# Optimization experiments

Measured on AMD Instinct MI355X. Metric: run time of the kernel, lower is better.

## Reference

```python
import jax, jax.numpy as jnp
import numpy as np

BATCH = 1_000_000
D = 20

def setup_inputs() -> dict:
    key = jax.random.key(0)
    kX, kW, kb, kR = jax.random.split(key, 4)
    X = jax.random.normal(kX, (BATCH, D), dtype=jnp.float32)
    W = jax.random.normal(kW, (D, D), dtype=jnp.float32)
    b = jax.random.normal(kb, (D,), dtype=jnp.float32)
    rand_weight = jax.random.uniform(kR, (D, D), dtype=jnp.float32)  # torch.rand, requires_grad=False
    return {"X": X, "W": W, "b": b, "rand_weight": rand_weight}

def reference(X, W, b, rand_weight):
    # X = self.linear(X)
    X1 = X @ W.T + b
    # X = relu(X @ rand_weight + 1)
    X2 = jax.nn.relu(X1 @ rand_weight + 1.0)
    # X = self.linear(X)  (shared weights)
    X3 = X2 @ W.T + b
    # while X.abs().sum() > 1: X = X / 2  -- data-dependent loop, kept on-device
    def cond(Xc):
        return jnp.sum(jnp.abs(Xc)) > 1.0
    def body(Xc):
        return Xc * 0.5
    Xf = jax.lax.while_loop(cond, body, X3)
    return jnp.sum(Xf)
```

## Files before the change

kernel.cpp:

```cpp
#include <hip/hip_runtime.h>
#include <math.h>

#define D 20
#define NROWS 1000000
#define NTILES (NROWS / 16)
#define TPB 256
#define MAIN_BLOCKS 1024
#define WAVES_TOTAL (MAIN_BLOCKS * (TPB/64))

typedef float  f32x4  __attribute__((ext_vector_type(4)));
typedef __bf16 bf16x8 __attribute__((ext_vector_type(8)));

#define FRAG_OFF (MAIN_BLOCKS * 2 * 8)

__device__ inline unsigned int pk2(float a, float b) {
  unsigned short la = __builtin_bit_cast(unsigned short, (__bf16)a);
  unsigned short lb = __builtin_bit_cast(unsigned short, (__bf16)b);
  return (unsigned int)la | ((unsigned int)lb << 16);
}

__global__ __launch_bounds__(512) void setup_kernel(
    const float* __restrict__ W, const float* __restrict__ b,
    const float* __restrict__ R, unsigned int* __restrict__ frags) {
  __shared__ float A_s[D * D];
  __shared__ float c_s[D];
  const int t = threadIdx.x;
  if (t < D * D) {
    int j = t / D, m = t % D;
    float s = 0.f;
#pragma unroll
    for (int i = 0; i < D; ++i) s = fmaf(W[i * D + j], R[i * D + m], s);
    A_s[j * D + m] = s;
  } else if (t < D * D + D) {
    int m = t - D * D;
    float s = 1.0f;
#pragma unroll
    for (int i = 0; i < D; ++i) s = fmaf(b[i], R[i * D + m], s);
    c_s[m] = s;
  }
  __syncthreads();
  if (t < 64) {
    const int G = t >> 4, ii = t & 15;
    uint4* out = (uint4*)frags;
    unsigned w[4];
    for (int wd = 0; wd < 4; ++wd) {
      float v[2];
      for (int h = 0; h < 2; ++h) {
        int k = G * 8 + 2 * wd + h;
        v[h] = (k < D) ? A_s[k * D + ii] : (k == D ? c_s[ii] : 0.f);
      }
      w[wd] = pk2(v[0], v[1]);
    }
    out[t] = make_uint4(w[0], w[1], w[2], w[3]);
    for (int wd = 0; wd < 4; ++wd) {
      float v[2];
      for (int h = 0; h < 2; ++h) {
        int k = G * 8 + 2 * wd + h;
        int m = 16 + ii;
        v[h] = (m < D) ? ((k < D) ? A_s[k * D + m] : (k == D ? c_s[m] : 0.f)) : 0.f;
      }
      w[wd] = pk2(v[0], v[1]);
    }
    out[64 + t] = make_uint4(w[0], w[1], w[2], w[3]);
    for (int wd = 0; wd < 4; ++wd) {
      float v[2];
      for (int h = 0; h < 2; ++h) {
        int e = 2 * wd + h;
        int sg = (e < 4) ? (4 * G + e) : (16 + 4 * G + (e - 4));
        v[h] = (sg < D) ? W[ii * D + sg] : (sg == D ? b[ii] : 0.f);
      }
      w[wd] = pk2(v[0], v[1]);
    }
    out[128 + t] = make_uint4(w[0], w[1], w[2], w[3]);
    for (int wd = 0; wd < 4; ++wd) {
      float v[2];
      for (int h = 0; h < 2; ++h) {
        int e = 2 * wd + h;
        int sg = (e < 4) ? (4 * G + e) : (16 + 4 * G + (e - 4));
        int n = 16 + ii;
        v[h] = (n < D) ? ((sg < D) ? W[n * D + sg] : (sg == D ? b[n] : 0.f)) : 0.f;
      }
      w[wd] = pk2(v[0], v[1]);
    }
    out[192 + t] = make_uint4(w[0], w[1], w[2], w[3]);
  }
}

__global__ __launch_bounds__(TPB) void main_kernel(
    const float* __restrict__ X, const unsigned int* __restrict__ frags,
    double* __restrict__ partial) {
  const int tid = threadIdx.x;
  const int lane = tid & 63;
  const int G = lane >> 4, ii = lane & 15;
  const int wid = tid >> 6;
  const int gwave = blockIdx.x * (TPB / 64) + wid;

  const uint4* fr = (const uint4*)frags;
  const bf16x8 B1t1 = __builtin_bit_cast(bf16x8, fr[lane]);
  const bf16x8 B1t2 = __builtin_bit_cast(bf16x8, fr[64 + lane]);
  const bf16x8 B2t1 = __builtin_bit_cast(bf16x8, fr[128 + lane]);
  const bf16x8 B2t2 = __builtin_bit_cast(bf16x8, fr[192 + lane]);

  const int g8 = (G < 2) ? G * 8 : 16;
  double s64 = 0.0, sa64 = 0.0;

  float4 xa = {0.f, 0.f, 0.f, 0.f}, xb = {0.f, 0.f, 0.f, 0.f};
  if (gwave < NTILES) {
    const float* p = X + (size_t)(gwave * 16 + ii) * D + g8;
    if (G < 3) xa = *(const float4*)p;
    if (G < 2) xb = *(const float4*)(p + 4);
  }

  for (int t = gwave; t < NTILES; t += WAVES_TOTAL) {
    const float4 ca = xa, cb = xb;
    const int tn = t + WAVES_TOTAL;
    xa = (float4){0.f, 0.f, 0.f, 0.f};
    xb = (float4){0.f, 0.f, 0.f, 0.f};
    if (tn < NTILES) {
      const float* p = X + (size_t)(tn * 16 + ii) * D + g8;
      if (G < 3) xa = *(const float4*)p;
      if (G < 2) xb = *(const float4*)(p + 4);
    }
    const float e4 = (G == 2) ? 1.0f : cb.x;
    bf16x8 xf;
    xf[0] = (__bf16)ca.x; xf[1] = (__bf16)ca.y;
    xf[2] = (__bf16)ca.z; xf[3] = (__bf16)ca.w;
    xf[4] = (__bf16)e4;   xf[5] = (__bf16)cb.y;
    xf[6] = (__bf16)cb.z; xf[7] = (__bf16)cb.w;

    const f32x4 zz = {0.f, 0.f, 0.f, 0.f};
    f32x4 a1 = __builtin_amdgcn_mfma_f32_16x16x32_bf16(B1t1, xf, zz, 0, 0, 0);
    f32x4 a2 = __builtin_amdgcn_mfma_f32_16x16x32_bf16(B1t2, xf, zz, 0, 0, 0);
#pragma unroll
    for (int q = 0; q < 4; ++q) {
      a1[q] = fmaxf(a1[q], 0.f);
      a2[q] = fmaxf(a2[q], 0.f);
    }
    const float hj = (G == 1) ? 1.0f : a2[0];
    bf16x8 x2f;
    x2f[0] = (__bf16)a1[0]; x2f[1] = (__bf16)a1[1];
    x2f[2] = (__bf16)a1[2]; x2f[3] = (__bf16)a1[3];
    x2f[4] = (__bf16)hj;    x2f[5] = (__bf16)a2[1];
    x2f[6] = (__bf16)a2[2]; x2f[7] = (__bf16)a2[3];

    f32x4 z1 = __builtin_amdgcn_mfma_f32_16x16x32_bf16(x2f, B2t1, zz, 0, 0, 0);
    f32x4 z2 = __builtin_amdgcn_mfma_f32_16x16x32_bf16(x2f, B2t2, zz, 0, 0, 0);

    const float s8 = ((z1[0] + z1[1]) + (z1[2] + z1[3])) +
                     ((z2[0] + z2[1]) + (z2[2] + z2[3]));
    const float sa8 = ((fabsf(z1[0]) + fabsf(z1[1])) + (fabsf(z1[2]) + fabsf(z1[3]))) +
                      ((fabsf(z2[0]) + fabsf(z2[1])) + (fabsf(z2[2]) + fabsf(z2[3])));
    s64 += (double)s8;
    sa64 += (double)sa8;
  }

#pragma unroll
  for (int off = 32; off > 0; off >>= 1) {
    s64 += __shfl_down(s64, off, 64);
    sa64 += __shfl_down(sa64, off, 64);
  }
  __shared__ double red[8];
  if ((tid & 63) == 0) { red[wid * 2] = s64; red[wid * 2 + 1] = sa64; }
  __syncthreads();
  if (tid == 0) {
    partial[2 * blockIdx.x]     = red[0] + red[2] + red[4] + red[6];
    partial[2 * blockIdx.x + 1] = red[1] + red[3] + red[5] + red[7];
  }
}

__global__ __launch_bounds__(256) void final_kernel(
    const double* __restrict__ partial, float* __restrict__ out) {
  double s = 0.0, sa = 0.0;
  for (int i = threadIdx.x; i < MAIN_BLOCKS; i += 256) {
    s += partial[2 * i];
    sa += partial[2 * i + 1];
  }
#pragma unroll
  for (int off = 32; off > 0; off >>= 1) {
    s += __shfl_down(s, off, 64);
    sa += __shfl_down(sa, off, 64);
  }
  __shared__ double red[8];
  int wid = threadIdx.x >> 6;
  if ((threadIdx.x & 63) == 0) { red[wid * 2] = s; red[wid * 2 + 1] = sa; }
  __syncthreads();
  if (threadIdx.x == 0) {
    double S  = red[0] + red[2] + red[4] + red[6];
    double SA = red[1] + red[3] + red[5] + red[7];
    int k = 0;
    double t = SA;
    while (t > 1.0 && k < 4096) { t *= 0.5; ++k; }
    out[0] = (float)ldexp(S, -k);
  }
}

extern "C" void kernel_launch(void* const* d_in, const int* in_sizes, int n_in,
                              void* d_out, int out_size, void* d_ws, size_t ws_size,
                              hipStream_t stream) {
  const float* X = (const float*)d_in[0];
  const float* W = (const float*)d_in[1];
  const float* b = (const float*)d_in[2];
  const float* R = (const float*)d_in[3];
  char* ws = (char*)d_ws;
  double* partial = (double*)ws;
  unsigned int* frags = (unsigned int*)(ws + FRAG_OFF);

  setup_kernel<<<1, 512, 0, stream>>>(W, b, R, frags);
  main_kernel<<<MAIN_BLOCKS, TPB, 0, stream>>>(X, frags, partial);
  final_kernel<<<1, 256, 0, stream>>>(partial, (float*)d_out);
}
```

Measured before the change: 30.38 us.

## Stage X tiles through shared memory with coalesced loads and many small blocks

Replaces the persistent grid-stride loop, which used strided per-lane float4 loads from global memory, with one block per 16-tile superblock. Each block first loads its contiguous chunk of X into LDS using fully coalesced float4 loads, then each wave processes 4 tiles from LDS. This aims to improve global-memory coalescing and bandwidth use. In exchange it launches about 3900 blocks, adds a barrier per block, uses LDS reads that may hit bank conflicts, and leaves more partials for the final reduction.

```diff
diff --git a/kernel.cpp b/kernel.cpp
--- a/kernel.cpp
+++ b/kernel.cpp
@@ -5,13 +5,15 @@
 #define NROWS 1000000
 #define NTILES (NROWS / 16)
 #define TPB 256
-#define MAIN_BLOCKS 1024
-#define WAVES_TOTAL (MAIN_BLOCKS * (TPB/64))
+#define TILES_PER_BLK 16
+#define NSB ((NTILES + TILES_PER_BLK - 1) / TILES_PER_BLK)
+#define NF4 (NROWS * D / 4)
+#define F4_PER_SB (TILES_PER_BLK * 16 * D / 4)
 
 typedef float  f32x4  __attribute__((ext_vector_type(4)));
 typedef __bf16 bf16x8 __attribute__((ext_vector_type(8)));
 
-#define FRAG_OFF (MAIN_BLOCKS * 2 * 8)
+#define FRAG_OFF 65536
 
 __device__ inline unsigned int pk2(float a, float b) {
   unsigned short la = __builtin_bit_cast(unsigned short, (__bf16)a);
@@ -89,69 +91,79 @@
 __global__ __launch_bounds__(TPB) void main_kernel(
     const float* __restrict__ X, const unsigned int* __restrict__ frags,
     double* __restrict__ partial) {
-  const int tid = threadIdx.x;
-  const int lane = tid & 63;
+  __shared__ float4 xs4[F4_PER_SB + 8];
+  float* xs = (float*)xs4;
+  const int t = threadIdx.x;
+  const int s = blockIdx.x;
+
+  const float4* X4 = (const float4*)X;
+#pragma unroll
+  for (int j = 0; j < 5; ++j) {
+    int gi = s * F4_PER_SB + j * TPB + t;
+    gi = (gi < NF4) ? gi : (NF4 - 1);
+    xs4[j * TPB + t] = X4[gi];
+  }
+
+  const int lane = t & 63;
   const int G = lane >> 4, ii = lane & 15;
-  const int wid = tid >> 6;
-  const int gwave = blockIdx.x * (TPB / 64) + wid;
-
+  const int wid = t >> 6;
   const uint4* fr = (const uint4*)frags;
   const bf16x8 B1t1 = __builtin_bit_cast(bf16x8, fr[lane]);
   const bf16x8 B1t2 = __builtin_bit_cast(bf16x8, fr[64 + lane]);
   const bf16x8 B2t1 = __builtin_bit_cast(bf16x8, fr[128 + lane]);
   const bf16x8 B2t2 = __builtin_bit_cast(bf16x8, fr[192 + lane]);
-
-  const int g8 = (G < 2) ? G * 8 : 16;
+  __syncthreads();
+
+  const bool mA = (G < 3);
+  const bool mB = (G < 2);
+  const int gf = (G < 2) ? G * 8 : 16;
+  const float* rowp = xs + ii * D + gf;
+  const int tbase = s * TILES_PER_BLK + wid * 4;
   double s64 = 0.0, sa64 = 0.0;
 
-  float4 xa = {0.f, 0.f, 0.f, 0.f}, xb = {0.f, 0.f, 0.f, 0.f};
-  if (gwave < NTILES) {
-    const float* p = X + (size_t)(gwave * 16 + ii) * D + g8;
-    if (G < 3) xa = *(const float4*)p;
-    if (G < 2) xb = *(const float4*)(p + 4);
-  }
-
-  for (int t = gwave; t < NTILES; t += WAVES_TOTAL) {
-    const float4 ca = xa, cb = xb;
-    const int tn = t + WAVES_TOTAL;
-    xa = (float4){0.f, 0.f, 0.f, 0.f};
-    xb = (float4){0.f, 0.f, 0.f, 0.f};
-    if (tn < NTILES) {
-      const float* p = X + (size_t)(tn * 16 + ii) * D + g8;
-      if (G < 3) xa = *(const float4*)p;
-      if (G < 2) xb = *(const float4*)(p + 4);
-    }
-    const float e4 = (G == 2) ? 1.0f : cb.x;
-    bf16x8 xf;
-    xf[0] = (__bf16)ca.x; xf[1] = (__bf16)ca.y;
-    xf[2] = (__bf16)ca.z; xf[3] = (__bf16)ca.w;
-    xf[4] = (__bf16)e4;   xf[5] = (__bf16)cb.y;
-    xf[6] = (__bf16)cb.z; xf[7] = (__bf16)cb.w;
-
-    const f32x4 zz = {0.f, 0.f, 0.f, 0.f};
-    f32x4 a1 = __builtin_amdgcn_mfma_f32_16x16x32_bf16(B1t1, xf, zz, 0, 0, 0);
-    f32x4 a2 = __builtin_amdgcn_mfma_f32_16x16x32_bf16(B1t2, xf, zz, 0, 0, 0);
-#pragma unroll
-    for (int q = 0; q < 4; ++q) {
-      a1[q] = fmaxf(a1[q], 0.f);
-      a2[q] = fmaxf(a2[q], 0.f);
-    }
-    const float hj = (G == 1) ? 1.0f : a2[0];
-    bf16x8 x2f;
-    x2f[0] = (__bf16)a1[0]; x2f[1] = (__bf16)a1[1];
-    x2f[2] = (__bf16)a1[2]; x2f[3] = (__bf16)a1[3];
-    x2f[4] = (__bf16)hj;    x2f[5] = (__bf16)a2[1];
-    x2f[6] = (__bf16)a2[2]; x2f[7] = (__bf16)a2[3];
-
-    f32x4 z1 = __builtin_amdgcn_mfma_f32_16x16x32_bf16(x2f, B2t1, zz, 0, 0, 0);
-    f32x4 z2 = __builtin_amdgcn_mfma_f32_16x16x32_bf16(x2f, B2t2, zz, 0, 0, 0);
-
-    const float s8 = ((z1[0] + z1[1]) + (z1[2] + z1[3])) +
-                     ((z2[0] + z2[1]) + (z2[2] + z2[3]));
-    const float sa8 = ((fabsf(z1[0]) + fabsf(z1[1])) + (fabsf(z1[2]) + fabsf(z1[3]))) +
-                      ((fabsf(z2[0]) + fabsf(z2[1])) + (fabsf(z2[2]) + fabsf(z2[3])));
-    s64 += (double)s8;
-    sa64 += (double)sa8;
+#pragma unroll
+  for (int k = 0; k < 4; ++k) {
+    if (tbase + k < NTILES) {
+      const float* p = rowp + (wid * 4 + k) * (16 * D);
+      const float4 ca = *(const float4*)p;
+      const float4 cb = *(const float4*)(p + 4);
+
+      bf16x8 xf;
+      xf[0] = (__bf16)(mA ? ca.x : 0.f);
+      xf[1] = (__bf16)(mA ? ca.y : 0.f);
+      xf[2] = (__bf16)(mA ? ca.z : 0.f);
+      xf[3] = (__bf16)(mA ? ca.w : 0.f);
+      xf[4] = (__bf16)(mB ? cb.x : (G == 2 ? 1.0f : 0.f));
+      xf[5] = (__bf16)(mB ? cb.y : 0.f);
+      xf[6] = (__bf16)(mB ? cb.z : 0.f);
+      xf[7] = (__bf16)(mB ? cb.w : 0.f);
+
+      const f32x4 zz = {0.f, 0.f, 0.f, 0.f};
+      f32x4 a1 = __builtin_amdgcn_mfma_f32_16x16x32_bf16(B1t1, xf, zz, 0, 0, 0);
+      f32x4 a2 = __builtin_amdgcn_mfma_f32_16x16x32_bf16(B1t2, xf, zz, 0, 0, 0);
+#pragma unroll
+      for (int q = 0; q < 4; ++q) {
+        a1[q] = fmaxf(a1[q], 0.f);
+        a2[q] = fmaxf(a2[q], 0.f);
+      }
+      const float hj = (G == 1) ? 1.0f : a2[0];
+      bf16x8 x2f;
+      x2f[0] = (__bf16)a1[0]; x2f[1] = (__bf16)a1[1];
+      x2f[2] = (__bf16)a1[2]; x2f[3] = (__bf16)a1[3];
+      x2f[4] = (__bf16)hj;    x2f[5] = (__bf16)a2[1];
+      x2f[6] = (__bf16)a2[2]; x2f[7] = (__bf16)a2[3];
+
+      f32x4 z1 = __builtin_amdgcn_mfma_f32_16x16x32_bf16(x2f, B2t1, zz, 0, 0, 0);
+      f32x4 z2 = __builtin_amdgcn_mfma_f32_16x16x32_bf16(x2f, B2t2, zz, 0, 0, 0);
+
+      const float s8 = ((z1[0] + z1[1]) + (z1[2] + z1[3])) +
+                       ((z2[0] + z2[1]) + (z2[2] + z2[3]));
+      const float sa8 =
+          ((fabsf(z1[0]) + fabsf(z1[1])) + (fabsf(z1[2]) + fabsf(z1[3]))) +
+          ((fabsf(z2[0]) + fabsf(z2[1])) + (fabsf(z2[2]) + fabsf(z2[3])));
+      s64 += (double)s8;
+      sa64 += (double)sa8;
+    }
   }
 
 #pragma unroll
@@ -160,18 +172,18 @@
     sa64 += __shfl_down(sa64, off, 64);
   }
   __shared__ double red[8];
-  if ((tid & 63) == 0) { red[wid * 2] = s64; red[wid * 2 + 1] = sa64; }
-  __syncthreads();
-  if (tid == 0) {
-    partial[2 * blockIdx.x]     = red[0] + red[2] + red[4] + red[6];
-    partial[2 * blockIdx.x + 1] = red[1] + red[3] + red[5] + red[7];
+  if ((t & 63) == 0) { red[wid * 2] = s64; red[wid * 2 + 1] = sa64; }
+  __syncthreads();
+  if (t == 0) {
+    partial[2 * s]     = red[0] + red[2] + red[4] + red[6];
+    partial[2 * s + 1] = red[1] + red[3] + red[5] + red[7];
   }
 }
 
 __global__ __launch_bounds__(256) void final_kernel(
     const double* __restrict__ partial, float* __restrict__ out) {
   double s = 0.0, sa = 0.0;
-  for (int i = threadIdx.x; i < MAIN_BLOCKS; i += 256) {
+  for (int i = threadIdx.x; i < NSB; i += 256) {
     s += partial[2 * i];
     sa += partial[2 * i + 1];
   }
@@ -206,6 +218,6 @@
   unsigned int* frags = (unsigned int*)(ws + FRAG_OFF);
 
   setup_kernel<<<1, 512, 0, stream>>>(W, b, R, frags);
-  main_kernel<<<MAIN_BLOCKS, TPB, 0, stream>>>(X, frags, partial);
+  main_kernel<<<NSB, TPB, 0, stream>>>(X, frags, partial);
   final_kernel<<<1, 256, 0, stream>>>(partial, (float*)d_out);
 }
```

Result: no change. 30.98 us (+2.0%).
